# Performance work log

Measured on AMD Instinct MI355X. Metric: run time of the kernel, lower is better.

The kernel has to match this reference:

```python
import jax, jax.numpy as jnp
import numpy as np

B, H, SEQLEN, HEAD_DIM = 1, 16, 4096, 64
SCALE = 1.0 / float(np.sqrt(HEAD_DIM))


def setup_inputs() -> dict:
    key = jax.random.key(0)
    kq, kk, kv = jax.random.split(key, 3)
    q = jax.random.normal(kq, (B, H, SEQLEN, HEAD_DIM), dtype=jnp.float32)
    k = jax.random.normal(kk, (B, H, HEAD_DIM, SEQLEN), dtype=jnp.float32)  # pre-transposed
    v = jax.random.normal(kv, (B, H, SEQLEN, HEAD_DIM), dtype=jnp.float32)
    return {"q": q, "k": k, "v": v}


def reference(q, k, v):
    # causal additive mask: -inf strictly above the diagonal
    mask = jnp.where(
        jnp.triu(jnp.ones((SEQLEN, SEQLEN), dtype=bool), k=1),
        jnp.float32(-jnp.inf), jnp.float32(0.0),
    ).astype(q.dtype)
    scores = jnp.einsum('bhsd,bhdt->bhst', q, k) * SCALE + mask  # [B,H,S,S]
    row_max = jnp.max(scores, axis=-1, keepdims=True)
    p_exp = jnp.exp(scores - row_max)
    denom = jnp.sum(p_exp, axis=-1, keepdims=True)
    p = p_exp / denom                                            # softmax probs
    out = jnp.einsum('bhst,bhtd->bhsd', p, v)                    # [B,H,S,D]
    row_sum = jnp.sum(p, axis=2)                                 # per-key accumulated attention [B,H,S]
    return (out, row_sum)
```

## Files before the change

kernel.cpp:

```cpp
#include <hip/hip_runtime.h>
#include <hip/hip_bf16.h>

#define HEADS 16
#define SEQ   4096
#define DIM   64
#define QT    64
#define KT    64
#define SCALE 0.125f
#define CF    0.18033688011112042f
#define LOG2E 1.4426950408889634f

typedef __bf16 v8bf  __attribute__((ext_vector_type(8)));
typedef __bf16 v4bf  __attribute__((ext_vector_type(4)));
typedef float  f32x4 __attribute__((ext_vector_type(4)));

__device__ __forceinline__ __bf16 to_bf(float f) { return (__bf16)f; }
__device__ __forceinline__ float ex2(float x) { return __builtin_amdgcn_exp2f(x); }
__device__ __forceinline__ float lg2(float x) { return __builtin_amdgcn_logf(x); }

__device__ __forceinline__ void gload16(const __bf16* g, __bf16* l) {
    __builtin_amdgcn_global_load_lds(
        (const __attribute__((address_space(1))) void*)g,
        (__attribute__((address_space(3))) void*)l,
        16, 0, 0);
}

__global__ __launch_bounds__(256) void conv_q_kernel(
    const float* __restrict__ qg, __bf16* __restrict__ Qb)
{
    size_t i = ((size_t)blockIdx.x * 256 + threadIdx.x) * 8;
    float4 f0 = *(const float4*)(qg + i);
    float4 f1 = *(const float4*)(qg + i + 4);
    v8bf o;
    o[0] = to_bf(f0.x * CF); o[1] = to_bf(f0.y * CF);
    o[2] = to_bf(f0.z * CF); o[3] = to_bf(f0.w * CF);
    o[4] = to_bf(f1.x * CF); o[5] = to_bf(f1.y * CF);
    o[6] = to_bf(f1.z * CF); o[7] = to_bf(f1.w * CF);
    *(v8bf*)(Qb + i) = o;
}

__global__ __launch_bounds__(256) void conv_kv_kernel(
    const float* __restrict__ kg, const float* __restrict__ vg,
    __bf16* __restrict__ Kb, __bf16* __restrict__ Vb)
{
    __shared__ __bf16 ldsT[64][65];
    const int h   = blockIdx.y;
    const int t0  = blockIdx.x * 64;
    const int tid = threadIdx.x;
    const int rr  = tid >> 2;
    const int cq  = (tid & 3) * 16;

    if (blockIdx.z == 0) {
        const float* src = kg + ((size_t)h * DIM + rr) * SEQ + t0 + cq;
        #pragma unroll
        for (int j = 0; j < 4; ++j) {
            float4 f = *(const float4*)(src + 4 * j);
            ldsT[rr][cq + 4 * j + 0] = to_bf(f.x);
            ldsT[rr][cq + 4 * j + 1] = to_bf(f.y);
            ldsT[rr][cq + 4 * j + 2] = to_bf(f.z);
            ldsT[rr][cq + 4 * j + 3] = to_bf(f.w);
        }
        __syncthreads();
        __bf16* dst = Kb + (size_t)h * SEQ * DIM + (size_t)(t0 + rr) * DIM + cq;
        v8bf o0, o1;
        #pragma unroll
        for (int i = 0; i < 8; ++i) {
            o0[i] = ldsT[cq + i][rr];
            o1[i] = ldsT[cq + 8 + i][rr];
        }
        *(v8bf*)dst = o0;
        *(v8bf*)(dst + 8) = o1;
    } else {
        const float* src = vg + ((size_t)h * SEQ + t0 + rr) * DIM + cq;
        #pragma unroll
        for (int j = 0; j < 4; ++j) {
            float4 f = *(const float4*)(src + 4 * j);
            ldsT[rr][cq + 4 * j + 0] = to_bf(f.x);
            ldsT[rr][cq + 4 * j + 1] = to_bf(f.y);
            ldsT[rr][cq + 4 * j + 2] = to_bf(f.z);
            ldsT[rr][cq + 4 * j + 3] = to_bf(f.w);
        }
        __syncthreads();
        __bf16* dst0 = Vb + ((size_t)h * DIM + rr) * SEQ + t0;
        const int n  = cq >> 4;
        const int c0 = 32 * (n >> 1) + 4 * (n & 1);
        #pragma unroll
        for (int j2 = 0; j2 < 4; ++j2) {
            v4bf ch;
            #pragma unroll
            for (int r = 0; r < 4; ++r)
                ch[r] = ldsT[cq + 4 * j2 + r][rr];
            *(v4bf*)(dst0 + c0 + 8 * j2) = ch;
        }
    }
}

__global__ __launch_bounds__(256, 4) void fa_fwd3_kernel(
    const __bf16* __restrict__ Qb, const __bf16* __restrict__ Kb,
    const __bf16* __restrict__ Vb, float* __restrict__ outg,
    float* __restrict__ lseg)
{
    const int b     = blockIdx.x;
    const int xcd   = b & 7;
    const int r     = b >> 3;
    const int h     = 2 * xcd + (r & 1);
    const int qtile = 63 - (r >> 1);
    const int tid   = threadIdx.x;
    const int wave  = tid >> 6;
    const int lane  = tid & 63;
    const int g     = lane >> 4;
    const int l16   = lane & 15;

    __shared__ alignas(16) __bf16 ldsK[2][KT * DIM];
    __shared__ alignas(16) __bf16 ldsV[2][DIM * KT];

    const int r0 = tid >> 3;
    const int c0 = tid & 7;
    const size_t kOff0 = (size_t)r0 * DIM + (size_t)((c0 ^ (r0 & 7)) << 3);
    const size_t kOff1 = (size_t)(r0 + 32) * DIM + (size_t)((c0 ^ ((r0 + 32) & 7)) << 3);
    const size_t vOff0 = (size_t)r0 * SEQ + (size_t)((c0 ^ (r0 & 7)) << 3);
    const size_t vOff1 = (size_t)(r0 + 32) * SEQ + (size_t)((c0 ^ ((r0 + 32) & 7)) << 3);
    const __bf16* KbH = Kb + (size_t)h * SEQ * DIM;
    const __bf16* VbH = Vb + (size_t)h * DIM * SEQ;
    const int ldsW = wave * 512;

    const int qw = qtile * QT + wave * 16;
    const int nt = qtile + 1;
    const int q  = qw + l16;

    const __bf16* qrow = Qb + ((size_t)h * SEQ + q) * DIM + g * 8;
    v8bf aq0 = *(const v8bf*)qrow;
    v8bf aq1 = *(const v8bf*)(qrow + 32);

    f32x4 acc[4];
    #pragma unroll
    for (int n = 0; n < 4; ++n) acc[n] = (f32x4){0.f, 0.f, 0.f, 0.f};
    float lp[4] = {0.f, 0.f, 0.f, 0.f};

    int cur = 0;
    gload16(KbH + kOff0, &ldsK[0][ldsW]);
    gload16(KbH + kOff1, &ldsK[0][2048 + ldsW]);
    gload16(VbH + vOff0, &ldsV[0][ldsW]);
    gload16(VbH + vOff1, &ldsV[0][2048 + ldsW]);
    __syncthreads();

    #pragma unroll 1
    for (int t = 0; t < nt; ++t) {
        if (t + 1 < nt) {
            const size_t kt = (size_t)(t + 1) * KT * DIM;
            const size_t vt = (size_t)(t + 1) * KT;
            gload16(KbH + kt + kOff0, &ldsK[cur ^ 1][ldsW]);
            gload16(KbH + kt + kOff1, &ldsK[cur ^ 1][2048 + ldsW]);
            gload16(VbH + vt + vOff0, &ldsV[cur ^ 1][ldsW]);
            gload16(VbH + vt + vOff1, &ldsV[cur ^ 1][2048 + ldsW]);
        }
        f32x4 s[4];
        #pragma unroll
        for (int n = 0; n < 4; ++n) s[n] = (f32x4){0.f, 0.f, 0.f, 0.f};
        __builtin_amdgcn_s_setprio(1);
        #pragma unroll
        for (int kk = 0; kk < 2; ++kk) {
            #pragma unroll
            for (int n = 0; n < 4; ++n) {
                int row  = 16 * n + l16;
                int byte = row * 128 + kk * 64 + g * 16;
                byte ^= (row & 7) << 4;
                v8bf ak = *(const v8bf*)&ldsK[cur][byte >> 1];
                s[n] = __builtin_amdgcn_mfma_f32_16x16x32_bf16(
                    ak, kk ? aq1 : aq0, s[n], 0, 0, 0);
            }
        }
        __builtin_amdgcn_s_setprio(0);
        if (t == nt - 1) {
            const int qit = wave * 16 + l16;
            #pragma unroll
            for (int n = 0; n < 4; ++n)
                #pragma unroll
                for (int r2 = 0; r2 < 4; ++r2)
                    if (16 * n + 4 * g + r2 > qit) s[n][r2] = -3.0e38f;
        }
        v8bf pa0, pa1;
        #pragma unroll
        for (int n = 0; n < 4; ++n) {
            #pragma unroll
            for (int r2 = 0; r2 < 4; ++r2) {
                float p = ex2(s[n][r2]);
                lp[r2] += p;
                if (n < 2) pa0[(n & 1) * 4 + r2] = to_bf(p);
                else       pa1[(n & 1) * 4 + r2] = to_bf(p);
            }
        }
        __builtin_amdgcn_s_setprio(1);
        #pragma unroll
        for (int kk = 0; kk < 2; ++kk) {
            #pragma unroll
            for (int n = 0; n < 4; ++n) {
                int row  = 16 * n + l16;
                int byte = row * 128 + kk * 64 + g * 16;
                byte ^= (row & 7) << 4;
                v8bf av = *(const v8bf*)&ldsV[cur][byte >> 1];
                acc[n] = __builtin_amdgcn_mfma_f32_16x16x32_bf16(
                    av, kk ? pa1 : pa0, acc[n], 0, 0, 0);
            }
        }
        __builtin_amdgcn_s_setprio(0);
        __syncthreads();
        cur ^= 1;
    }

    float l = (lp[0] + lp[1]) + (lp[2] + lp[3]);
    l += __shfl_xor(l, 16);
    l += __shfl_xor(l, 32);
    const float inv = 1.0f / l;
    float* orow = outg + ((size_t)h * SEQ + q) * DIM;
    #pragma unroll
    for (int n = 0; n < 4; ++n) {
        f32x4 o = acc[n];
        o[0] *= inv; o[1] *= inv; o[2] *= inv; o[3] *= inv;
        *(f32x4*)(orow + 16 * n + 4 * g) = o;
    }
    if (g == 0)
        lseg[h * SEQ + q] = lg2(l);
}

__global__ __launch_bounds__(256, 4) void fa_colsum2_kernel(
    const __bf16* __restrict__ Qb, const __bf16* __restrict__ Kb,
    const float* __restrict__ lseg, float* __restrict__ partg)
{
    const int b    = blockIdx.x;
    const int xcd  = b & 7;
    const int j    = b >> 3;
    const int h    = 2 * xcd + (j & 1);
    const int m    = j >> 1;
    const int ta   = m & 31;
    const int half = m >> 5;
    const int tb   = 63 - ta;
    const int smid = (ta <= 15) ? (ta + 33) : 48;
    const int qlo  = half ? smid : ta;
    const int qhiE = half ? 64 : smid;
    const int tid  = threadIdx.x;
    const int wave = tid >> 6;
    const int lane = tid & 63;
    const int g    = lane >> 4;
    const int l16  = lane & 15;

    __shared__ alignas(16) __bf16 ldsK2[2][KT * DIM];
    __shared__ float cs[2][4][KT];

    const int r0 = tid >> 3;
    const int c0 = tid & 7;
    const size_t kOff0 = (size_t)r0 * DIM + (size_t)((c0 ^ (r0 & 7)) << 3);
    const size_t kOff1 = (size_t)(r0 + 32) * DIM + (size_t)((c0 ^ ((r0 + 32) & 7)) << 3);
    const __bf16* KbH = Kb + (size_t)h * SEQ * DIM;
    const int ldsW = wave * 512;

    gload16(KbH + (size_t)ta * KT * DIM + kOff0, &ldsK2[0][ldsW]);
    gload16(KbH + (size_t)ta * KT * DIM + kOff1, &ldsK2[0][2048 + ldsW]);
    gload16(KbH + (size_t)tb * KT * DIM + kOff0, &ldsK2[1][ldsW]);
    gload16(KbH + (size_t)tb * KT * DIM + kOff1, &ldsK2[1][2048 + ldsW]);
    __syncthreads();

    float accA[4] = {0.f, 0.f, 0.f, 0.f};
    float accB[4] = {0.f, 0.f, 0.f, 0.f};

    #pragma unroll 1
    for (int qt = qlo; qt < qhiE; ++qt) {
        const int qw = qt * QT + wave * 16;
        const __bf16* qrow = Qb + ((size_t)h * SEQ + qw + l16) * DIM + g * 8;
        v8bf aq0 = *(const v8bf*)qrow;
        v8bf aq1 = *(const v8bf*)(qrow + 32);
        float4 lse4 = *(const float4*)(lseg + (size_t)h * SEQ + qw + 4 * g);

        {
            f32x4 s[4];
            #pragma unroll
            for (int n = 0; n < 4; ++n) s[n] = (f32x4){0.f, 0.f, 0.f, 0.f};
            __builtin_amdgcn_s_setprio(1);
            #pragma unroll
            for (int kk = 0; kk < 2; ++kk)
                #pragma unroll
                for (int n = 0; n < 4; ++n) {
                    int row  = 16 * n + l16;
                    int byte = row * 128 + kk * 64 + g * 16;
                    byte ^= (row & 7) << 4;
                    v8bf bk = *(const v8bf*)&ldsK2[0][byte >> 1];
                    s[n] = __builtin_amdgcn_mfma_f32_16x16x32_bf16(
                        kk ? aq1 : aq0, bk, s[n], 0, 0, 0);
                }
            __builtin_amdgcn_s_setprio(0);
            if (qt == ta) {
                #pragma unroll
                for (int n = 0; n < 4; ++n) {
                    const int key = ta * KT + 16 * n + l16;
                    #pragma unroll
                    for (int r2 = 0; r2 < 4; ++r2) {
                        float e = ex2(s[n][r2] - lse4[r2]);
                        accA[n] += (key <= qw + 4 * g + r2) ? e : 0.f;
                    }
                }
            } else {
                #pragma unroll
                for (int n = 0; n < 4; ++n)
                    #pragma unroll
                    for (int r2 = 0; r2 < 4; ++r2)
                        accA[n] += ex2(s[n][r2] - lse4[r2]);
            }
        }
        if (qt >= tb) {
            f32x4 s[4];
            #pragma unroll
            for (int n = 0; n < 4; ++n) s[n] = (f32x4){0.f, 0.f, 0.f, 0.f};
            __builtin_amdgcn_s_setprio(1);
            #pragma unroll
            for (int kk = 0; kk < 2; ++kk)
                #pragma unroll
                for (int n = 0; n < 4; ++n) {
                    int row  = 16 * n + l16;
                    int byte = row * 128 + kk * 64 + g * 16;
                    byte ^= (row & 7) << 4;
                    v8bf bk = *(const v8bf*)&ldsK2[1][byte >> 1];
                    s[n] = __builtin_amdgcn_mfma_f32_16x16x32_bf16(
                        kk ? aq1 : aq0, bk, s[n], 0, 0, 0);
                }
            __builtin_amdgcn_s_setprio(0);
            if (qt == tb) {
                #pragma unroll
                for (int n = 0; n < 4; ++n) {
                    const int key = tb * KT + 16 * n + l16;
                    #pragma unroll
                    for (int r2 = 0; r2 < 4; ++r2) {
                        float e = ex2(s[n][r2] - lse4[r2]);
                        accB[n] += (key <= qw + 4 * g + r2) ? e : 0.f;
                    }
                }
            } else {
                #pragma unroll
                for (int n = 0; n < 4; ++n)
                    #pragma unroll
                    for (int r2 = 0; r2 < 4; ++r2)
                        accB[n] += ex2(s[n][r2] - lse4[r2]);
            }
        }
    }

    #pragma unroll
    for (int n = 0; n < 4; ++n) {
        accA[n] += __shfl_xor(accA[n], 16);
        accA[n] += __shfl_xor(accA[n], 32);
        accB[n] += __shfl_xor(accB[n], 16);
        accB[n] += __shfl_xor(accB[n], 32);
    }
    if (lane < 16) {
        #pragma unroll
        for (int n = 0; n < 4; ++n) {
            cs[0][wave][16 * n + lane] = accA[n];
            cs[1][wave][16 * n + lane] = accB[n];
        }
    }
    __syncthreads();
    float* pg = partg + (size_t)half * HEADS * SEQ + (size_t)h * SEQ;
    if (tid < KT) {
        pg[ta * KT + tid] =
            cs[0][0][tid] + cs[0][1][tid] + cs[0][2][tid] + cs[0][3][tid];
    } else if (tid < 2 * KT) {
        const int t = tid - KT;
        pg[tb * KT + t] =
            cs[1][0][t] + cs[1][1][t] + cs[1][2][t] + cs[1][3][t];
    }
}

__global__ __launch_bounds__(256) void rs_add_kernel(
    const float* __restrict__ partg, float* __restrict__ rsg)
{
    const int i = blockIdx.x * 256 + threadIdx.x;
    f32x4 x = *(const f32x4*)(partg + (size_t)i * 4);
    f32x4 y = *(const f32x4*)(partg + (size_t)HEADS * SEQ + (size_t)i * 4);
    x[0] += y[0]; x[1] += y[1]; x[2] += y[2]; x[3] += y[3];
    *(f32x4*)(rsg + (size_t)i * 4) = x;
}

__global__ __launch_bounds__(256, 1) void fa_fwd_v1_kernel(
    const float* __restrict__ qg, const float* __restrict__ kg,
    const float* __restrict__ vg, float* __restrict__ outg,
    float* __restrict__ lseg)
{
    const int h    = blockIdx.y;
    const int q0   = blockIdx.x * QT;
    const int tid  = threadIdx.x;
    const int wave = tid >> 6;
    const int lane = tid & 63;
    const int g    = lane >> 4;
    const int l16  = lane & 15;

    __shared__ alignas(16) __bf16 ldsK[KT * DIM];
    __shared__ alignas(16) __bf16 ldsV[DIM * KT];
    __shared__ alignas(16) __bf16 ldsP[4][16 * 72];

    const int qw = q0 + wave * 16;
    v8bf aq[2];
    {
        const float* qrow = qg + ((size_t)h * SEQ + qw + l16) * DIM;
        #pragma unroll
        for (int kk = 0; kk < 2; ++kk) {
            const float* p = qrow + kk * 32 + g * 8;
            float4 f0 = *(const float4*)p;
            float4 f1 = *(const float4*)(p + 4);
            aq[kk][0] = to_bf(f0.x); aq[kk][1] = to_bf(f0.y);
            aq[kk][2] = to_bf(f0.z); aq[kk][3] = to_bf(f0.w);
            aq[kk][4] = to_bf(f1.x); aq[kk][5] = to_bf(f1.y);
            aq[kk][6] = to_bf(f1.z); aq[kk][7] = to_bf(f1.w);
        }
    }
    f32x4 acc[4];
    #pragma unroll
    for (int n = 0; n < 4; ++n) acc[n] = (f32x4){0.f, 0.f, 0.f, 0.f};
    float m_r[4], l_r[4];
    #pragma unroll
    for (int r = 0; r < 4; ++r) { m_r[r] = -__builtin_inff(); l_r[r] = 0.f; }

    const int ntiles = q0 / KT + 1;
    const int kd = tid >> 2;
    const int kc = (tid & 3) * 16;

    for (int t = 0; t < ntiles; ++t) {
        const int t0 = t * KT;
        __syncthreads();
        {
            const float* src = kg + ((size_t)h * DIM + kd) * SEQ + t0 + kc;
            #pragma unroll
            for (int j = 0; j < 4; ++j) {
                float4 f = *(const float4*)(src + 4 * j);
                #pragma unroll
                for (int i = 0; i < 4; ++i) {
                    int row  = kc + 4 * j + i;
                    int byte = row * 128 + kd * 2;
                    byte ^= (row & 7) << 4;
                    ldsK[byte >> 1] = to_bf(((const float*)&f)[i]);
                }
            }
        }
        {
            const float* src = vg + ((size_t)h * SEQ + t0 + kd) * DIM + kc;
            #pragma unroll
            for (int j = 0; j < 4; ++j) {
                float4 f = *(const float4*)(src + 4 * j);
                #pragma unroll
                for (int i = 0; i < 4; ++i) {
                    int row  = kc + 4 * j + i;
                    int byte = row * 128 + kd * 2;
                    byte ^= (row & 7) << 4;
                    ldsV[byte >> 1] = to_bf(((const float*)&f)[i]);
                }
            }
        }
        __syncthreads();

        f32x4 s[4];
        #pragma unroll
        for (int n = 0; n < 4; ++n) s[n] = (f32x4){0.f, 0.f, 0.f, 0.f};
        #pragma unroll
        for (int kk = 0; kk < 2; ++kk)
            #pragma unroll
            for (int n = 0; n < 4; ++n) {
                int row  = 16 * n + l16;
                int byte = row * 128 + kk * 64 + g * 16;
                byte ^= (row & 7) << 4;
                v8bf bk = *(const v8bf*)&ldsK[byte >> 1];
                s[n] = __builtin_amdgcn_mfma_f32_16x16x32_bf16(aq[kk], bk, s[n], 0, 0, 0);
            }
        float pvv[4][4];
        #pragma unroll
        for (int r = 0; r < 4; ++r) {
            const int qq = qw + 4 * g + r;
            float sv[4];
            #pragma unroll
            for (int n = 0; n < 4; ++n) {
                int key = t0 + 16 * n + l16;
                sv[n] = (key <= qq) ? s[n][r] * (SCALE * LOG2E) : -3.0e38f;
            }
            float mx = fmaxf(fmaxf(sv[0], sv[1]), fmaxf(sv[2], sv[3]));
            mx = fmaxf(mx, __shfl_xor(mx, 1));
            mx = fmaxf(mx, __shfl_xor(mx, 2));
            mx = fmaxf(mx, __shfl_xor(mx, 4));
            mx = fmaxf(mx, __shfl_xor(mx, 8));
            float mnew = fmaxf(m_r[r], mx);
            float corr = ex2(m_r[r] - mnew);
            m_r[r] = mnew;
            float rs = 0.f;
            #pragma unroll
            for (int n = 0; n < 4; ++n) {
                float p = (sv[n] > -1.0e38f) ? ex2(sv[n] - mnew) : 0.f;
                pvv[n][r] = p;
                rs += p;
            }
            rs += __shfl_xor(rs, 1);
            rs += __shfl_xor(rs, 2);
            rs += __shfl_xor(rs, 4);
            rs += __shfl_xor(rs, 8);
            l_r[r] = l_r[r] * corr + rs;
            #pragma unroll
            for (int n = 0; n < 4; ++n) acc[n][r] *= corr;
        }
        #pragma unroll
        for (int n = 0; n < 4; ++n)
            #pragma unroll
            for (int r = 0; r < 4; ++r)
                ldsP[wave][(4 * g + r) * 72 + 16 * n + l16] = to_bf(pvv[n][r]);
        asm volatile("s_waitcnt lgkmcnt(0)" ::: "memory");
        __builtin_amdgcn_sched_barrier(0);
        #pragma unroll
        for (int kk = 0; kk < 2; ++kk) {
            v8bf ap = *(const v8bf*)&ldsP[wave][l16 * 72 + 32 * kk + 8 * g];
            #pragma unroll
            for (int n = 0; n < 4; ++n) {
                int row  = 16 * n + l16;
                int byte = row * 128 + kk * 64 + g * 16;
                byte ^= (row & 7) << 4;
                v8bf bv = *(const v8bf*)&ldsV[byte >> 1];
                acc[n] = __builtin_amdgcn_mfma_f32_16x16x32_bf16(ap, bv, acc[n], 0, 0, 0);
            }
        }
    }
    #pragma unroll
    for (int r = 0; r < 4; ++r) {
        const int qq  = qw + 4 * g + r;
        const float inv = 1.0f / l_r[r];
        float* orow = outg + ((size_t)h * SEQ + qq) * DIM;
        #pragma unroll
        for (int n = 0; n < 4; ++n)
            orow[16 * n + l16] = acc[n][r] * inv;
        if (l16 == 0)
            lseg[h * SEQ + qq] = m_r[r] + lg2(l_r[r]);
    }
}

__global__ __launch_bounds__(256, 1) void fa_colsum_v1_kernel(
    const float* __restrict__ qg, const float* __restrict__ kg,
    const float* __restrict__ lseg, float* __restrict__ rsg)
{
    const int h    = blockIdx.y;
    const int t0   = blockIdx.x * KT;
    const int tid  = threadIdx.x;
    const int wave = tid >> 6;
    const int lane = tid & 63;
    const int g    = lane >> 4;
    const int l16  = lane & 15;

    __shared__ alignas(16) __bf16 ldsK[KT * DIM];
    __shared__ float cs[4][KT];
    {
        const int kd = tid >> 2;
        const int kc = (tid & 3) * 16;
        const float* src = kg + ((size_t)h * DIM + kd) * SEQ + t0 + kc;
        #pragma unroll
        for (int j = 0; j < 4; ++j) {
            float4 f = *(const float4*)(src + 4 * j);
            #pragma unroll
            for (int i = 0; i < 4; ++i) {
                int row  = kc + 4 * j + i;
                int byte = row * 128 + kd * 2;
                byte ^= (row & 7) << 4;
                ldsK[byte >> 1] = to_bf(((const float*)&f)[i]);
            }
        }
    }
    __syncthreads();
    float colacc[4] = {0.f, 0.f, 0.f, 0.f};
    for (int qt = t0 / QT; qt < SEQ / QT; ++qt) {
        const int qw = qt * QT + wave * 16;
        const float* qrow = qg + ((size_t)h * SEQ + qw + l16) * DIM;
        v8bf aq[2];
        #pragma unroll
        for (int kk = 0; kk < 2; ++kk) {
            const float* p = qrow + kk * 32 + g * 8;
            float4 f0 = *(const float4*)p;
            float4 f1 = *(const float4*)(p + 4);
            aq[kk][0] = to_bf(f0.x); aq[kk][1] = to_bf(f0.y);
            aq[kk][2] = to_bf(f0.z); aq[kk][3] = to_bf(f0.w);
            aq[kk][4] = to_bf(f1.x); aq[kk][5] = to_bf(f1.y);
            aq[kk][6] = to_bf(f1.z); aq[kk][7] = to_bf(f1.w);
        }
        float lse_r[4];
        #pragma unroll
        for (int r = 0; r < 4; ++r)
            lse_r[r] = lseg[h * SEQ + qw + 4 * g + r];
        f32x4 s[4];
        #pragma unroll
        for (int n = 0; n < 4; ++n) s[n] = (f32x4){0.f, 0.f, 0.f, 0.f};
        #pragma unroll
        for (int kk = 0; kk < 2; ++kk)
            #pragma unroll
            for (int n = 0; n < 4; ++n) {
                int row  = 16 * n + l16;
                int byte = row * 128 + kk * 64 + g * 16;
                byte ^= (row & 7) << 4;
                v8bf bk = *(const v8bf*)&ldsK[byte >> 1];
                s[n] = __builtin_amdgcn_mfma_f32_16x16x32_bf16(aq[kk], bk, s[n], 0, 0, 0);
            }
        #pragma unroll
        for (int n = 0; n < 4; ++n) {
            const int key = t0 + 16 * n + l16;
            #pragma unroll
            for (int r = 0; r < 4; ++r) {
                const int qq = qw + 4 * g + r;
                if (key <= qq)
                    colacc[n] += ex2(s[n][r] * (SCALE * LOG2E) - lse_r[r]);
            }
        }
    }
    #pragma unroll
    for (int n = 0; n < 4; ++n) {
        colacc[n] += __shfl_xor(colacc[n], 16);
        colacc[n] += __shfl_xor(colacc[n], 32);
    }
    if (lane < 16) {
        #pragma unroll
        for (int n = 0; n < 4; ++n)
            cs[wave][16 * n + lane] = colacc[n];
    }
    __syncthreads();
    if (tid < KT) {
        float v = cs[0][tid] + cs[1][tid] + cs[2][tid] + cs[3][tid];
        rsg[h * SEQ + t0 + tid] = v;
    }
}

extern "C" void kernel_launch(void* const* d_in, const int* in_sizes, int n_in,
                              void* d_out, int out_size, void* d_ws, size_t ws_size,
                              hipStream_t stream) {
    (void)in_sizes; (void)n_in; (void)out_size;
    const float* qg = (const float*)d_in[0];
    const float* kg = (const float*)d_in[1];
    const float* vg = (const float*)d_in[2];
    float* outg = (float*)d_out;
    float* rsg  = outg + (size_t)HEADS * SEQ * DIM;

    const size_t nElem   = (size_t)HEADS * SEQ * DIM;
    const size_t lseB    = (size_t)HEADS * SEQ * sizeof(float);
    const size_t needB   = lseB + 3 * nElem * sizeof(__bf16);

    if (ws_size >= needB) {
        float*  lseg = (float*)d_ws;
        __bf16* Qb = (__bf16*)((char*)d_ws + lseB);
        __bf16* Kb = Qb + nElem;
        __bf16* Vb = Kb + nElem;
        float* partg = (float*)Vb;
        conv_q_kernel<<<dim3((int)(nElem / 2048)), 256, 0, stream>>>(qg, Qb);
        conv_kv_kernel<<<dim3(SEQ / 64, HEADS, 2), 256, 0, stream>>>(kg, vg, Kb, Vb);
        fa_fwd3_kernel<<<dim3(1024), 256, 0, stream>>>(Qb, Kb, Vb, outg, lseg);
        fa_colsum2_kernel<<<dim3(1024), 256, 0, stream>>>(Qb, Kb, lseg, partg);
        rs_add_kernel<<<dim3(HEADS * SEQ / 1024), 256, 0, stream>>>(partg, rsg);
    } else {
        float* lseg = (float*)d_ws;
        dim3 grid(SEQ / QT, HEADS);
        fa_fwd_v1_kernel<<<grid, 256, 0, stream>>>(qg, kg, vg, outg, lseg);
        fa_colsum_v1_kernel<<<grid, 256, 0, stream>>>(qg, kg, lseg, rsg);
    }
}
```

Before: 113.6 us.

## Pair causal q-tiles per block and triple-buffer K/V loads with explicit waitcnt

```diff
diff --git a/kernel.cpp b/kernel.cpp
--- a/kernel.cpp
+++ b/kernel.cpp
@@ -95,24 +95,24 @@
     }
 }
 
-__global__ __launch_bounds__(256, 4) void fa_fwd3_kernel(
+__global__ __launch_bounds__(256, 2) void fa_fwd4_kernel(
     const __bf16* __restrict__ Qb, const __bf16* __restrict__ Kb,
     const __bf16* __restrict__ Vb, float* __restrict__ outg,
     float* __restrict__ lseg)
 {
-    const int b     = blockIdx.x;
-    const int xcd   = b & 7;
-    const int r     = b >> 3;
-    const int h     = 2 * xcd + (r & 1);
-    const int qtile = 63 - (r >> 1);
-    const int tid   = threadIdx.x;
-    const int wave  = tid >> 6;
-    const int lane  = tid & 63;
-    const int g     = lane >> 4;
-    const int l16   = lane & 15;
-
-    __shared__ alignas(16) __bf16 ldsK[2][KT * DIM];
-    __shared__ alignas(16) __bf16 ldsV[2][DIM * KT];
+    const int b    = blockIdx.x;
+    const int xcd  = b & 7;
+    const int j    = b >> 3;
+    const int h    = 2 * xcd + (j & 1);
+    const int bq   = j >> 1;
+    const int tid  = threadIdx.x;
+    const int wave = tid >> 6;
+    const int lane = tid & 63;
+    const int g    = lane >> 4;
+    const int l16  = lane & 15;
+
+    __shared__ alignas(16) __bf16 ldsK[3][KT * DIM];
+    __shared__ alignas(16) __bf16 ldsV[3][DIM * KT];
 
     const int r0 = tid >> 3;
     const int c0 = tid & 7;
@@ -124,103 +124,127 @@
     const __bf16* VbH = Vb + (size_t)h * DIM * SEQ;
     const int ldsW = wave * 512;
 
-    const int qw = qtile * QT + wave * 16;
-    const int nt = qtile + 1;
-    const int q  = qw + l16;
-
-    const __bf16* qrow = Qb + ((size_t)h * SEQ + q) * DIM + g * 8;
-    v8bf aq0 = *(const v8bf*)qrow;
-    v8bf aq1 = *(const v8bf*)(qrow + 32);
-
-    f32x4 acc[4];
-    #pragma unroll
-    for (int n = 0; n < 4; ++n) acc[n] = (f32x4){0.f, 0.f, 0.f, 0.f};
-    float lp[4] = {0.f, 0.f, 0.f, 0.f};
-
-    int cur = 0;
-    gload16(KbH + kOff0, &ldsK[0][ldsW]);
-    gload16(KbH + kOff1, &ldsK[0][2048 + ldsW]);
-    gload16(VbH + vOff0, &ldsV[0][ldsW]);
-    gload16(VbH + vOff1, &ldsV[0][2048 + ldsW]);
-    __syncthreads();
-
     #pragma unroll 1
-    for (int t = 0; t < nt; ++t) {
-        if (t + 1 < nt) {
-            const size_t kt = (size_t)(t + 1) * KT * DIM;
-            const size_t vt = (size_t)(t + 1) * KT;
-            gload16(KbH + kt + kOff0, &ldsK[cur ^ 1][ldsW]);
-            gload16(KbH + kt + kOff1, &ldsK[cur ^ 1][2048 + ldsW]);
-            gload16(VbH + vt + vOff0, &ldsV[cur ^ 1][ldsW]);
-            gload16(VbH + vt + vOff1, &ldsV[cur ^ 1][2048 + ldsW]);
-        }
-        f32x4 s[4];
-        #pragma unroll
-        for (int n = 0; n < 4; ++n) s[n] = (f32x4){0.f, 0.f, 0.f, 0.f};
-        __builtin_amdgcn_s_setprio(1);
-        #pragma unroll
-        for (int kk = 0; kk < 2; ++kk) {
+    for (int pi = 0; pi < 2; ++pi) {
+        const int qtile = pi ? (63 - bq) : bq;
+        const int qw = qtile * QT + wave * 16;
+        const int nt = qtile + 1;
+        const int q  = qw + l16;
+
+        const __bf16* qrow = Qb + ((size_t)h * SEQ + q) * DIM + g * 8;
+        v8bf aq0 = *(const v8bf*)qrow;
+        v8bf aq1 = *(const v8bf*)(qrow + 32);
+
+        f32x4 acc[4];
+        #pragma unroll
+        for (int n = 0; n < 4; ++n) acc[n] = (f32x4){0.f, 0.f, 0.f, 0.f};
+        float lp[4] = {0.f, 0.f, 0.f, 0.f};
+
+        {
+            gload16(KbH + kOff0, &ldsK[0][ldsW]);
+            gload16(KbH + kOff1, &ldsK[0][2048 + ldsW]);
+            gload16(VbH + vOff0, &ldsV[0][ldsW]);
+            gload16(VbH + vOff1, &ldsV[0][2048 + ldsW]);
+            if (nt > 1) {
+                const __bf16* kb = KbH + (size_t)KT * DIM;
+                const __bf16* vb = VbH + KT;
+                gload16(kb + kOff0, &ldsK[1][ldsW]);
+                gload16(kb + kOff1, &ldsK[1][2048 + ldsW]);
+                gload16(vb + vOff0, &ldsV[1][ldsW]);
+                gload16(vb + vOff1, &ldsV[1][2048 + ldsW]);
+            }
+        }
+
+        int bi = 0;
+        int si = 2;
+
+        #pragma unroll 1
+        for (int t = 0; t < nt; ++t) {
+            if (t + 1 < nt) {
+                asm volatile("s_waitcnt vmcnt(4)" ::: "memory");
+            } else {
+                asm volatile("s_waitcnt vmcnt(0)" ::: "memory");
+            }
+            __builtin_amdgcn_sched_barrier(0);
+            __builtin_amdgcn_s_barrier();
+            __builtin_amdgcn_sched_barrier(0);
+            if (t + 2 < nt) {
+                const __bf16* kb = KbH + (size_t)(t + 2) * KT * DIM;
+                const __bf16* vb = VbH + (size_t)(t + 2) * KT;
+                gload16(kb + kOff0, &ldsK[si][ldsW]);
+                gload16(kb + kOff1, &ldsK[si][2048 + ldsW]);
+                gload16(vb + vOff0, &ldsV[si][ldsW]);
+                gload16(vb + vOff1, &ldsV[si][2048 + ldsW]);
+            }
+            f32x4 s[4];
+            #pragma unroll
+            for (int n = 0; n < 4; ++n) s[n] = (f32x4){0.f, 0.f, 0.f, 0.f};
+            __builtin_amdgcn_s_setprio(1);
+            #pragma unroll
+            for (int kk = 0; kk < 2; ++kk) {
+                #pragma unroll
+                for (int n = 0; n < 4; ++n) {
+                    int row  = 16 * n + l16;
+                    int byte = row * 128 + kk * 64 + g * 16;
+                    byte ^= (row & 7) << 4;
+                    v8bf ak = *(const v8bf*)&ldsK[bi][byte >> 1];
+                    s[n] = __builtin_amdgcn_mfma_f32_16x16x32_bf16(
+                        ak, kk ? aq1 : aq0, s[n], 0, 0, 0);
+                }
+            }
+            __builtin_amdgcn_s_setprio(0);
+            if (t == nt - 1) {
+                const int qit = wave * 16 + l16;
+                #pragma unroll
+                for (int n = 0; n < 4; ++n)
+                    #pragma unroll
+                    for (int r2 = 0; r2 < 4; ++r2)
+                        if (16 * n + 4 * g + r2 > qit) s[n][r2] = -3.0e38f;
+            }
+            v8bf pa0, pa1;
             #pragma unroll
             for (int n = 0; n < 4; ++n) {
-                int row  = 16 * n + l16;
-                int byte = row * 128 + kk * 64 + g * 16;
-                byte ^= (row & 7) << 4;
-                v8bf ak = *(const v8bf*)&ldsK[cur][byte >> 1];
-                s[n] = __builtin_amdgcn_mfma_f32_16x16x32_bf16(
-                    ak, kk ? aq1 : aq0, s[n], 0, 0, 0);
-            }
-        }
-        __builtin_amdgcn_s_setprio(0);
-        if (t == nt - 1) {
-            const int qit = wave * 16 + l16;
-            #pragma unroll
-            for (int n = 0; n < 4; ++n)
-                #pragma unroll
-                for (int r2 = 0; r2 < 4; ++r2)
-                    if (16 * n + 4 * g + r2 > qit) s[n][r2] = -3.0e38f;
-        }
-        v8bf pa0, pa1;
+                #pragma unroll
+                for (int r2 = 0; r2 < 4; ++r2) {
+                    float p = ex2(s[n][r2]);
+                    lp[r2] += p;
+                    if (n < 2) pa0[(n & 1) * 4 + r2] = to_bf(p);
+                    else       pa1[(n & 1) * 4 + r2] = to_bf(p);
+                }
+            }
+            __builtin_amdgcn_s_setprio(1);
+            #pragma unroll
+            for (int kk = 0; kk < 2; ++kk) {
+                #pragma unroll
+                for (int n = 0; n < 4; ++n) {
+                    int row  = 16 * n + l16;
+                    int byte = row * 128 + kk * 64 + g * 16;
+                    byte ^= (row & 7) << 4;
+                    v8bf av = *(const v8bf*)&ldsV[bi][byte >> 1];
+                    acc[n] = __builtin_amdgcn_mfma_f32_16x16x32_bf16(
+                        av, kk ? pa1 : pa0, acc[n], 0, 0, 0);
+                }
+            }
+            __builtin_amdgcn_s_setprio(0);
+            bi = (bi == 2) ? 0 : bi + 1;
+            si = (si == 2) ? 0 : si + 1;
+        }
+        __builtin_amdgcn_s_barrier();
+
+        float l = (lp[0] + lp[1]) + (lp[2] + lp[3]);
+        l += __shfl_xor(l, 16);
+        l += __shfl_xor(l, 32);
+        const float inv = 1.0f / l;
+        float* orow = outg + ((size_t)h * SEQ + q) * DIM;
         #pragma unroll
         for (int n = 0; n < 4; ++n) {
-            #pragma unroll
-            for (int r2 = 0; r2 < 4; ++r2) {
-                float p = ex2(s[n][r2]);
-                lp[r2] += p;
-                if (n < 2) pa0[(n & 1) * 4 + r2] = to_bf(p);
-                else       pa1[(n & 1) * 4 + r2] = to_bf(p);
-            }
-        }
-        __builtin_amdgcn_s_setprio(1);
-        #pragma unroll
-        for (int kk = 0; kk < 2; ++kk) {
-            #pragma unroll
-            for (int n = 0; n < 4; ++n) {
-                int row  = 16 * n + l16;
-                int byte = row * 128 + kk * 64 + g * 16;
-                byte ^= (row & 7) << 4;
-                v8bf av = *(const v8bf*)&ldsV[cur][byte >> 1];
-                acc[n] = __builtin_amdgcn_mfma_f32_16x16x32_bf16(
-                    av, kk ? pa1 : pa0, acc[n], 0, 0, 0);
-            }
-        }
-        __builtin_amdgcn_s_setprio(0);
-        __syncthreads();
-        cur ^= 1;
-    }
-
-    float l = (lp[0] + lp[1]) + (lp[2] + lp[3]);
-    l += __shfl_xor(l, 16);
-    l += __shfl_xor(l, 32);
-    const float inv = 1.0f / l;
-    float* orow = outg + ((size_t)h * SEQ + q) * DIM;
-    #pragma unroll
-    for (int n = 0; n < 4; ++n) {
-        f32x4 o = acc[n];
-        o[0] *= inv; o[1] *= inv; o[2] *= inv; o[3] *= inv;
-        *(f32x4*)(orow + 16 * n + 4 * g) = o;
-    }
-    if (g == 0)
-        lseg[h * SEQ + q] = lg2(l);
+            f32x4 o = acc[n];
+            o[0] *= inv; o[1] *= inv; o[2] *= inv; o[3] *= inv;
+            *(f32x4*)(orow + 16 * n + 4 * g) = o;
+        }
+        if (g == 0)
+            lseg[h * SEQ + q] = lg2(l);
+    }
 }
 
 __global__ __launch_bounds__(256, 4) void fa_colsum2_kernel(
@@ -647,7 +671,7 @@
         float* partg = (float*)Vb;
         conv_q_kernel<<<dim3((int)(nElem / 2048)), 256, 0, stream>>>(qg, Qb);
         conv_kv_kernel<<<dim3(SEQ / 64, HEADS, 2), 256, 0, stream>>>(kg, vg, Kb, Vb);
-        fa_fwd3_kernel<<<dim3(1024), 256, 0, stream>>>(Qb, Kb, Vb, outg, lseg);
+        fa_fwd4_kernel<<<dim3(512), 256, 0, stream>>>(Qb, Kb, Vb, outg, lseg);
         fa_colsum2_kernel<<<dim3(1024), 256, 0, stream>>>(Qb, Kb, lseg, partg);
         rs_add_kernel<<<dim3(HEADS * SEQ / 1024), 256, 0, stream>>>(partg, rsg);
     } else {
```

Measured after the change: 118.0 us. 1.04x slower.
